# Performance work log

Hardware: AMD Instinct MI355X
Metric: run time of the kernel (lower is better)

Reference implementation:

```python
import jax, jax.numpy as jnp
import numpy as np

B, L, H, V = 16, 1024, 512, 32000
HALF = H // 2
ALPHA = 0.95
EPS_NORM = 1e-12
EPS_LN = 1e-5


def setup_inputs() -> dict:
    key = jax.random.key(0)
    ks = jax.random.split(key, 12)
    s = 0.02
    return {
        "seq": jax.random.randint(ks[0], (B, L), 0, V),
        "embed": jax.random.normal(ks[1], (V, H), jnp.float32) * s,
        "ff_w1": jax.random.normal(ks[2], (2 * H, H), jnp.float32) * s,
        "ff_b1": jnp.zeros((2 * H,), jnp.float32),
        "ff_w2": jax.random.normal(ks[3], (H, 2 * H), jnp.float32) * s,
        "ff_b2": jnp.zeros((H,), jnp.float32),
        "gamma": jnp.ones((H,), jnp.float32),
        "beta": jnp.zeros((H,), jnp.float32),
        "sem_w": jax.random.normal(ks[4], (HALF, H), jnp.float32) * s,
        "epi_w": jax.random.normal(ks[5], (HALF, H), jnp.float32) * s,
        "rp_w": jax.random.normal(ks[6], (H, H), jnp.float32) * s,
        "rp_b": jnp.zeros((H,), jnp.float32),
        "out_w": jax.random.normal(ks[7], (V, H), jnp.float32) * s,
        "out_b": jnp.zeros((V,), jnp.float32),
    }


def _layernorm(x, gamma, beta):
    mu = jnp.mean(x, axis=-1, keepdims=True)
    var = jnp.mean(jnp.square(x - mu), axis=-1, keepdims=True)
    return (x - mu) * jax.lax.rsqrt(var + EPS_LN) * gamma + beta


def _l2norm(k):
    # F.normalize: k / max(||k||_2, eps)
    n = jnp.sqrt(jnp.sum(jnp.square(k), axis=-1, keepdims=True))
    return k / jnp.maximum(n, EPS_NORM)


def reference(seq, embed, ff_w1, ff_b1, ff_w2, ff_b2, gamma, beta,
              sem_w, epi_w, rp_w, rp_b, out_w, out_b):
    h = embed[seq]  # [B, L, H]
    ff = jnp.maximum(jnp.einsum('blh,fh->blf', h, ff_w1) + ff_b1, 0.0)
    ff = jnp.einsum('blf,hf->blh', ff, ff_w2) + ff_b2
    h = _layernorm(h + ff, gamma, beta)  # [B, L, H]

    # precompute all keys, time-major for scan: [L, B, half]
    ks_all = jnp.einsum('blh,ch->lbc', h, sem_w)
    ke_all = jnp.einsum('blh,ch->lbc', h, epi_w)

    def step(carry, inp):
        Ms, Me = carry                      # [B, half, half]
        ks, ke = inp                        # [B, half]
        kns = _l2norm(ks)
        kne = _l2norm(ke)
        vps = jnp.einsum('bij,bj->bi', Ms, kns)
        vpe = jnp.einsum('bij,bj->bi', Me, kne)
        Ds = (ks - vps)[:, :, None] * kns[:, None, :]
        De = (ke - vpe)[:, :, None] * kne[:, None, :]
        Ms = Ms + (1.0 - ALPHA) * Ds
        Me = Me + (1.0 - ALPHA) * De
        return (Ms, Me), None

    M0 = jnp.zeros((B, HALF, HALF), h.dtype)
    (M_s, M_e), _ = jax.lax.scan(step, (M0, M0), (ks_all[:L - 1], ke_all[:L - 1]))

    qs = ks_all[L - 1]  # sem_p(h[:, -1])
    qe = ke_all[L - 1]  # epi_p(h[:, -1])
    cs = jnp.einsum('bij,bj->bi', M_s, qs)
    ce = jnp.einsum('bij,bj->bi', M_e, qe)
    c = jnp.concatenate([cs, ce], axis=-1)  # [B, H]
    r = jnp.einsum('bh,gh->bg', c, rp_w) + rp_b
    return jnp.einsum('bh,vh->bv', r, out_w) + out_b  # [B, V]
```

## Files before the change

### kernel.cpp

```cpp
#include <hip/hip_runtime.h>
#include <stdint.h>

#define Bsz 16
#define Lsz 1024
#define Hsz 512
#define Vsz 32000
#define HALF 256
#define BETA 0.05f

typedef unsigned short u16;
typedef __attribute__((ext_vector_type(8))) short short8;
typedef __attribute__((ext_vector_type(4))) float f32x4;

__device__ __forceinline__ float bf2f(u16 u) { return __uint_as_float(((unsigned int)u) << 16); }
__device__ __forceinline__ u16 f2bf(float f) {
    unsigned int u = __float_as_uint(f);
    return (u16)((u + 0x7FFFu + ((u >> 16) & 1u)) >> 16);
}
__device__ __forceinline__ u16 f2h(float f) {
    _Float16 h = (_Float16)f;
    return *(u16*)&h;
}
__device__ __forceinline__ bool mode_f32(const void* gamma) {
    return *(const unsigned int*)gamma == 0x3F800000u;
}

__device__ __forceinline__ float wave_sum(float p) {
    p += __shfl_xor(p, 32, 64);
    p += __shfl_xor(p, 16, 64);
    p += __shfl_xor(p, 8, 64);
    p += __shfl_xor(p, 4, 64);
    p += __shfl_xor(p, 2, 64);
    p += __shfl_xor(p, 1, 64);
    return p;
}

__device__ __forceinline__ void cvt8(const void* src, u16* dst, int i, bool f32m) {
    union { u16 u[8]; uint4 q; } o;
    if (f32m) {
        const float* s = (const float*)src + i;
        const float4 a = *(const float4*)s;
        const float4 b = *(const float4*)(s + 4);
        o.u[0] = f2bf(a.x); o.u[1] = f2bf(a.y); o.u[2] = f2bf(a.z); o.u[3] = f2bf(a.w);
        o.u[4] = f2bf(b.x); o.u[5] = f2bf(b.y); o.u[6] = f2bf(b.z); o.u[7] = f2bf(b.w);
    } else {
        o.q = *(const uint4*)((const u16*)src + i);
    }
    *(uint4*)(dst + i) = o.q;
}

__global__ __launch_bounds__(256)
void cvt_all(const void* s0, const void* s1, const void* s2, const void* s3,
             const void* s4, const void* s5, const void* s6, const void* s7,
             const void* s8, const void* s9, const void* s10,
             u16* d0, u16* d1, u16* d2, u16* d3, u16* d4, u16* d5, u16* d6,
             u16* d7, u16* d8, u16* d9, u16* d10, const void* gamma) {
    const bool f32m = mode_f32(gamma);
    const int g = blockIdx.x * 256 + threadIdx.x;
    const void* src; u16* dst; int off;
    if      (g < 65536)  { src = s0;  dst = d0;  off = g; }
    else if (g < 131072) { src = s1;  dst = d1;  off = g - 65536; }
    else if (g < 147456) { src = s2;  dst = d2;  off = g - 131072; }
    else if (g < 163840) { src = s3;  dst = d3;  off = g - 147456; }
    else if (g < 196608) { src = s4;  dst = d4;  off = g - 163840; }
    else if (g < 196736) { src = s5;  dst = d5;  off = g - 196608; }
    else if (g < 196800) { src = s6;  dst = d6;  off = g - 196736; }
    else if (g < 196864) { src = s7;  dst = d7;  off = g - 196800; }
    else if (g < 196928) { src = s8;  dst = d8;  off = g - 196864; }
    else if (g < 196992) { src = s9;  dst = d9;  off = g - 196928; }
    else if (g < 200992) { src = s10; dst = d10; off = g - 196992; }
    else return;
    cvt8(src, dst, off * 8, f32m);
}

__global__ __launch_bounds__(256)
void gather_kernel(const int* __restrict__ seq, const void* __restrict__ embed,
                   u16* __restrict__ h0, const void* __restrict__ gamma) {
    const bool f32m = mode_f32(gamma);
    const int row = blockIdx.x * 4 + (threadIdx.x >> 6);
    const int lane = threadIdx.x & 63;
    const int tok = seq[row];
    union { u16 u[8]; uint4 q; } o;
    if (f32m) {
        const float* e = (const float*)embed + (size_t)tok * Hsz + lane * 8;
        const float4 a = *(const float4*)e;
        const float4 b = *(const float4*)(e + 4);
        o.u[0] = f2bf(a.x); o.u[1] = f2bf(a.y); o.u[2] = f2bf(a.z); o.u[3] = f2bf(a.w);
        o.u[4] = f2bf(b.x); o.u[5] = f2bf(b.y); o.u[6] = f2bf(b.z); o.u[7] = f2bf(b.w);
    } else {
        o.q = *((const uint4*)((const u16*)embed + (size_t)tok * Hsz) + lane);
    }
    *((uint4*)(h0 + (size_t)row * Hsz) + lane) = o.q;
}

template <int EPI>
__global__ __launch_bounds__(256)
void gemm128(const u16* __restrict__ A, const u16* __restrict__ B0,
             const u16* __restrict__ B1, const u16* __restrict__ bias,
             const u16* resid, void* Cout, u16* __restrict__ kT,
             int M, int N, int K) {
    __shared__ u16 Als[128 * 32];
    __shared__ u16 Bls[128 * 32];
    const int tid = threadIdx.x;
    const int wave = tid >> 6, lane = tid & 63;
    const int m0 = blockIdx.y * 128, n0 = blockIdx.x * 128;

    const u16* Bt;
    if (EPI == 2) Bt = (n0 < HALF) ? (B0 + (size_t)n0 * K) : (B1 + (size_t)(n0 - HALF) * K);
    else          Bt = B0 + (size_t)n0 * K;
    const u16* At = A + (size_t)m0 * K;

    const int wm = wave >> 1, wn = wave & 1;
    const int srow = lane >> 2;
    const int sk = (lane & 3) * 8;
    const int fr = lane & 15;
    const int fq = (lane >> 4) * 8;

    f32x4 acc[4][4];
#pragma unroll
    for (int i = 0; i < 4; i++)
#pragma unroll
        for (int j = 0; j < 4; j++) acc[i][j] = (f32x4){0.f, 0.f, 0.f, 0.f};

    for (int k0 = 0; k0 < K; k0 += 32) {
        __syncthreads();
#pragma unroll
        for (int c = 0; c < 2; c++) {
            const int ch = wave * 2 + c;
            const int row = ch * 16 + srow;
            __builtin_amdgcn_global_load_lds(
                (const __attribute__((address_space(1))) uint32_t*)(At + (size_t)row * K + k0 + sk),
                (__attribute__((address_space(3))) uint32_t*)(&Als[ch * 512]), 16, 0, 0);
            __builtin_amdgcn_global_load_lds(
                (const __attribute__((address_space(1))) uint32_t*)(Bt + (size_t)row * K + k0 + sk),
                (__attribute__((address_space(3))) uint32_t*)(&Bls[ch * 512]), 16, 0, 0);
        }
        __syncthreads();
        short8 af[4], bfr[4];
#pragma unroll
        for (int i = 0; i < 4; i++)
            af[i] = *(const short8*)&Als[(wm * 64 + i * 16 + fr) * 32 + fq];
#pragma unroll
        for (int j = 0; j < 4; j++)
            bfr[j] = *(const short8*)&Bls[(wn * 64 + j * 16 + fr) * 32 + fq];
#pragma unroll
        for (int i = 0; i < 4; i++)
#pragma unroll
            for (int j = 0; j < 4; j++)
                acc[i][j] = __builtin_amdgcn_mfma_f32_16x16x32_bf16(af[i], bfr[j], acc[i][j], 0, 0, 0);
    }

#pragma unroll
    for (int i = 0; i < 4; i++) {
#pragma unroll
        for (int j = 0; j < 4; j++) {
            const int n = n0 + wn * 64 + j * 16 + fr;
            if (EPI == 2) {
                const int mbase = m0 + wm * 64 + i * 16 + (lane >> 4) * 4;
                const int mem = n >> 8, col = n & 255;
                const int b = mbase >> 10, t0 = mbase & 1023;
                u16 tv[4];
#pragma unroll
                for (int r = 0; r < 4; r++) {
                    const int t = t0 + r;
                    const u16 bv = f2bf(acc[i][j][r]);
                    tv[r] = bv;
                    ((u16*)Cout)[((size_t)(mem * Bsz + b) * Lsz + t) * HALF + col] = bv;
                }
                *(uint2*)&kT[((size_t)(mem * Bsz + b) * HALF + col) * Lsz + t0] = *(uint2*)tv;
            } else {
#pragma unroll
                for (int r = 0; r < 4; r++) {
                    const int m = m0 + wm * 64 + i * 16 + (lane >> 4) * 4 + r;
                    float v = acc[i][j][r];
                    if (EPI == 0) {
                        v += bf2f(bias[n]);
                        v = v > 0.f ? v : 0.f;
                        ((u16*)Cout)[(size_t)m * N + n] = f2bf(v);
                    } else {
                        v += bf2f(bias[n]) + bf2f(resid[(size_t)m * N + n]);
                        ((u16*)Cout)[(size_t)m * N + n] = f2bf(v);
                    }
                }
            }
        }
    }
}

__global__ __launch_bounds__(256)
void ln_kernel(const u16* hs, const u16* __restrict__ gamma,
               const u16* __restrict__ beta, u16* hn) {
    const int row = blockIdx.x * 4 + (threadIdx.x >> 6);
    const int lane = threadIdx.x & 63;
    const uint4 raw = *(const uint4*)(hs + (size_t)row * Hsz + lane * 8);
    const u16* xr = (const u16*)&raw;
    float v[8];
#pragma unroll
    for (int j = 0; j < 8; j++) v[j] = bf2f(xr[j]);
    float s = 0.f;
#pragma unroll
    for (int j = 0; j < 8; j++) s += v[j];
    s = wave_sum(s);
    const float mu = s * (1.f / 512.f);
    float q = 0.f;
#pragma unroll
    for (int j = 0; j < 8; j++) { v[j] -= mu; q += v[j] * v[j]; }
    q = wave_sum(q);
    const float rstd = rsqrtf(q * (1.f / 512.f) + 1e-5f);
    union { u16 u[8]; uint4 qv; } o;
#pragma unroll
    for (int j = 0; j < 8; j++) {
        const int n = lane * 8 + j;
        o.u[j] = f2bf(v[j] * rstd * bf2f(gamma[n]) + bf2f(beta[n]));
    }
    *(uint4*)(hn + (size_t)row * Hsz + lane * 8) = o.qv;
}

__global__ __launch_bounds__(256)
void normalize_kernel(u16* kb, float* __restrict__ norms, float* __restrict__ invs) {
    const int row = blockIdx.x * 4 + (threadIdx.x >> 6);
    const int lane = threadIdx.x & 63;
    u16* p = kb + (size_t)row * HALF + lane * 4;
    uint2 raw = *(uint2*)p;
    const u16* kp = (const u16*)&raw;
    float f[4];
#pragma unroll
    for (int j = 0; j < 4; j++) f[j] = bf2f(kp[j]);
    float s = f[0]*f[0] + f[1]*f[1] + f[2]*f[2] + f[3]*f[3];
    s = wave_sum(s);
    const float n = fmaxf(sqrtf(s), 1e-12f);
    const float inv = 1.f / n;
    union { u16 u[4]; uint2 q; } o;
#pragma unroll
    for (int j = 0; j < 4; j++) o.u[j] = f2bf(f[j] * inv);
    *(uint2*)p = o.q;
    if (lane == 0) { norms[row] = n; invs[row] = inv; }
}

__global__ __launch_bounds__(256)
void gramsolve_kernel(const u16* __restrict__ kn, u16* __restrict__ W) {
    __shared__ u16 ls[64 * 264];
    __shared__ float Gl[64 * 64];
    const int mb = blockIdx.x, c = blockIdx.y;
    const int tid = threadIdx.x;
    const u16* src = kn + ((size_t)mb * Lsz + c * 64) * HALF;
    {
        const int row = tid >> 2, p = tid & 3;
        const u16* sp = src + row * 256 + p * 64;
        u16* dp = ls + row * 264 + p * 64;
#pragma unroll
        for (int i = 0; i < 8; i++)
            *(uint4*)(dp + i * 8) = *(const uint4*)(sp + i * 8);
    }
    __syncthreads();
    const int wave = tid >> 6, lane = tid & 63;
    const int fr = lane & 15, fq = (lane >> 4) * 8;
    f32x4 acc[4];
#pragma unroll
    for (int j = 0; j < 4; j++) acc[j] = (f32x4){0.f, 0.f, 0.f, 0.f};
    for (int k0 = 0; k0 < 256; k0 += 32) {
        const short8 a = *(const short8*)&ls[(wave * 16 + fr) * 264 + k0 + fq];
#pragma unroll
        for (int j = 0; j < 4; j++) {
            const short8 b = *(const short8*)&ls[(j * 16 + fr) * 264 + k0 + fq];
            acc[j] = __builtin_amdgcn_mfma_f32_16x16x32_bf16(a, b, acc[j], 0, 0, 0);
        }
    }
#pragma unroll
    for (int j = 0; j < 4; j++)
#pragma unroll
        for (int r = 0; r < 4; r++)
            Gl[(wave * 16 + (lane >> 4) * 4 + r) * 64 + j * 16 + fr] = acc[j][r];
    __syncthreads();

    u16* Wc = W + (((size_t)mb * 16 + c) * 64) * HALF;
    const bool last = (c == 15);
    float w[64];
#pragma unroll
    for (int t = 63; t >= 0; --t) {
        float a0 = 0.f, a1 = 0.f, a2 = 0.f, a3 = 0.f;
        const int q0 = (t + 4) & ~3;
#pragma unroll
        for (int tp = t + 1; tp < q0; ++tp) a0 += Gl[t * 64 + tp] * w[tp];
#pragma unroll
        for (int q = q0; q < 64; q += 4) {
            const f32x4 g = *(const f32x4*)&Gl[t * 64 + q];
            a0 += g[0] * w[q];     a1 += g[1] * w[q + 1];
            a2 += g[2] * w[q + 2]; a3 += g[3] * w[q + 3];
        }
        float wt = bf2f(ls[t * 264 + tid]) - BETA * ((a0 + a1) + (a2 + a3));
        if (last && t == 63) wt = 0.f;
        w[t] = wt;
        Wc[t * HALF + tid] = f2h(wt);
    }
}

__global__ __launch_bounds__(256, 1)
void scan3_kernel(const u16* __restrict__ kn, const u16* __restrict__ kT,
                  const float* __restrict__ norms, const float* __restrict__ invs,
                  const u16* __restrict__ W, float* __restrict__ cbuf) {
    __shared__ float uL[256], suL[64], scL[64];
    const int mb = blockIdx.x;
    const int tid = threadIdx.x;
    const int t = tid >> 2, p = tid & 3;
    const float* nb = norms + (size_t)mb * Lsz;
    const float* ib = invs + (size_t)mb * Lsz;

    float u = bf2f(kn[((size_t)mb * Lsz + 1023) * HALF + tid]) * nb[1023];
    float cacc = 0.f;
    uL[tid] = u;

    const u16* kTrow = kT + ((size_t)mb * HALF + tid) * Lsz;
    const u16* Wrow = W + (size_t)mb * 16 * 64 * HALF + (size_t)t * HALF + (size_t)p * 64;

    uint4 wA[8], kA[8], wB[8], kB[8];
    {
        const u16* wp = Wrow + (size_t)15 * 64 * HALF;
        const u16* kp = kTrow + 15 * 64;
#pragma unroll
        for (int i = 0; i < 8; i++) wA[i] = *(const uint4*)(wp + i * 8);
#pragma unroll
        for (int i = 0; i < 8; i++) kA[i] = *(const uint4*)(kp + i * 8);
    }
    asm volatile("s_waitcnt lgkmcnt(0)" ::: "memory");
    __builtin_amdgcn_s_barrier();

    auto process = [&](const uint4 (&WR)[8], const uint4 (&KQ)[8], const int c) {
        {
            float pa = 0.f, pb = 0.f;
#pragma unroll
            for (int i = 0; i < 8; i++) {
                union { uint4 q; _Float16 h[8]; } wv; wv.q = WR[i];
                const f32x4 u0 = *(const f32x4*)&uL[p * 64 + i * 8];
                const f32x4 u1 = *(const f32x4*)&uL[p * 64 + i * 8 + 4];
                pa += (float)wv.h[0] * u0[0] + (float)wv.h[1] * u0[1]
                    + (float)wv.h[2] * u0[2] + (float)wv.h[3] * u0[3];
                pb += (float)wv.h[4] * u1[0] + (float)wv.h[5] * u1[1]
                    + (float)wv.h[6] * u1[2] + (float)wv.h[7] * u1[3];
            }
            float part = pa + pb;
            part += __shfl_xor(part, 1, 64);
            part += __shfl_xor(part, 2, 64);
            if (p == 0) { suL[t] = part * ib[c * 64 + t]; scL[t] = part; }
        }
        asm volatile("s_waitcnt lgkmcnt(0)" ::: "memory");
        __builtin_amdgcn_s_barrier();
        {
            float du0 = 0.f, du1 = 0.f, dc0 = 0.f, dc1 = 0.f;
#pragma unroll
            for (int i = 0; i < 8; i++) {
                const u16* kk = (const u16*)&KQ[i];
                const f32x4 sa = *(const f32x4*)&suL[i * 8];
                const f32x4 sb = *(const f32x4*)&suL[i * 8 + 4];
                const f32x4 ca = *(const f32x4*)&scL[i * 8];
                const f32x4 cb = *(const f32x4*)&scL[i * 8 + 4];
                const float k0 = bf2f(kk[0]), k1 = bf2f(kk[1]);
                const float k2 = bf2f(kk[2]), k3 = bf2f(kk[3]);
                const float k4 = bf2f(kk[4]), k5 = bf2f(kk[5]);
                const float k6 = bf2f(kk[6]), k7 = bf2f(kk[7]);
                du0 += sa[0] * k0 + sa[1] * k1 + sa[2] * k2 + sa[3] * k3;
                du1 += sb[0] * k4 + sb[1] * k5 + sb[2] * k6 + sb[3] * k7;
                dc0 += ca[0] * k0 + ca[1] * k1 + ca[2] * k2 + ca[3] * k3;
                dc1 += cb[0] * k4 + cb[1] * k5 + cb[2] * k6 + cb[3] * k7;
            }
            u -= BETA * (du0 + du1);
            cacc += BETA * (dc0 + dc1);
            uL[tid] = u;
        }
        asm volatile("s_waitcnt lgkmcnt(0)" ::: "memory");
        __builtin_amdgcn_s_barrier();
    };

    for (int cc = 15; cc >= 1; cc -= 2) {
        {
            const u16* wp = Wrow + (size_t)(cc - 1) * 64 * HALF;
            const u16* kp = kTrow + (cc - 1) * 64;
#pragma unroll
            for (int i = 0; i < 8; i++) wB[i] = *(const uint4*)(wp + i * 8);
#pragma unroll
            for (int i = 0; i < 8; i++) kB[i] = *(const uint4*)(kp + i * 8);
        }
        __builtin_amdgcn_sched_barrier(0);
        process(wA, kA, cc);
        if (cc >= 3) {
            const u16* wp = Wrow + (size_t)(cc - 2) * 64 * HALF;
            const u16* kp = kTrow + (cc - 2) * 64;
#pragma unroll
            for (int i = 0; i < 8; i++) wA[i] = *(const uint4*)(wp + i * 8);
#pragma unroll
            for (int i = 0; i < 8; i++) kA[i] = *(const uint4*)(kp + i * 8);
        }
        __builtin_amdgcn_sched_barrier(0);
        process(wB, kB, cc - 1);
    }
    const int b = mb & 15, mem = mb >> 4;
    cbuf[(size_t)b * Hsz + mem * HALF + tid] = cacc;
}

__global__ __launch_bounds__(256)
void rproj_kernel(const float* __restrict__ cbuf, const u16* __restrict__ rpw,
                  const u16* __restrict__ rpb, u16* __restrict__ rbuf) {
    __shared__ float cl[Hsz];
    const int b = blockIdx.x, tid = threadIdx.x;
    cl[tid] = cbuf[(size_t)b * Hsz + tid];
    cl[tid + 256] = cbuf[(size_t)b * Hsz + 256 + tid];
    __syncthreads();
#pragma unroll
    for (int gg = 0; gg < 2; gg++) {
        const int g = gg * 256 + tid;
        const u16* wr = rpw + (size_t)g * Hsz;
        float acc = bf2f(rpb[g]);
        for (int k = 0; k < Hsz; k += 8) {
            const uint4 w8 = *(const uint4*)(wr + k);
            const u16* w = (const u16*)&w8;
            const float4 c0 = *(const float4*)&cl[k];
            const float4 c1 = *(const float4*)&cl[k + 4];
            acc += bf2f(w[0]) * c0.x + bf2f(w[1]) * c0.y + bf2f(w[2]) * c0.z + bf2f(w[3]) * c0.w
                 + bf2f(w[4]) * c1.x + bf2f(w[5]) * c1.y + bf2f(w[6]) * c1.z + bf2f(w[7]) * c1.w;
        }
        rbuf[(size_t)b * Hsz + g] = f2bf(acc);
    }
}

__global__ __launch_bounds__(256)
void logits_kernel(const u16* __restrict__ rbuf, const void* __restrict__ outw,
                   const u16* __restrict__ outb, void* __restrict__ out,
                   const void* __restrict__ gamma) {
    __shared__ u16 rls[16 * Hsz];
    const bool f32m = mode_f32(gamma);
    const int tid = threadIdx.x;
    {
        const uint4* src = (const uint4*)rbuf;
        uint4* dst = (uint4*)rls;
#pragma unroll
        for (int i = 0; i < 4; i++) dst[i * 256 + tid] = src[i * 256 + tid];
    }
    __syncthreads();
    const int wave = tid >> 6, lane = tid & 63;
    const int n0 = blockIdx.x * 256 + wave * 64;
    const int fr = lane & 15, fq = (lane >> 4) * 8;
    f32x4 acc[4];
#pragma unroll
    for (int j = 0; j < 4; j++) acc[j] = (f32x4){0.f, 0.f, 0.f, 0.f};
    if (f32m) {
        for (int k0 = 0; k0 < Hsz; k0 += 32) {
            const short8 af = *(const short8*)&rls[fr * Hsz + k0 + fq];
#pragma unroll
            for (int j = 0; j < 4; j++) {
                const float* wp = (const float*)outw + (size_t)(n0 + j * 16 + fr) * Hsz + k0 + fq;
                const float4 a = *(const float4*)wp;
                const float4 bq = *(const float4*)(wp + 4);
                union { u16 u[8]; short8 v; } bb;
                bb.u[0] = f2bf(a.x); bb.u[1] = f2bf(a.y); bb.u[2] = f2bf(a.z); bb.u[3] = f2bf(a.w);
                bb.u[4] = f2bf(bq.x); bb.u[5] = f2bf(bq.y); bb.u[6] = f2bf(bq.z); bb.u[7] = f2bf(bq.w);
                acc[j] = __builtin_amdgcn_mfma_f32_16x16x32_bf16(af, bb.v, acc[j], 0, 0, 0);
            }
        }
    } else {
        for (int k0 = 0; k0 < Hsz; k0 += 32) {
            const short8 af = *(const short8*)&rls[fr * Hsz + k0 + fq];
#pragma unroll
            for (int j = 0; j < 4; j++) {
                const short8 b8 = *(const short8*)((const u16*)outw + (size_t)(n0 + j * 16 + fr) * Hsz + k0 + fq);
                acc[j] = __builtin_amdgcn_mfma_f32_16x16x32_bf16(af, b8, acc[j], 0, 0, 0);
            }
        }
    }
#pragma unroll
    for (int j = 0; j < 4; j++) {
        const int v = n0 + j * 16 + fr;
        const float bv = bf2f(outb[v]);
#pragma unroll
        for (int r = 0; r < 4; r++) {
            const int bb = (lane >> 4) * 4 + r;
            const float val = acc[j][r] + bv;
            if (f32m) ((float*)out)[(size_t)bb * Vsz + v] = val;
            else      ((u16*)out)[(size_t)bb * Vsz + v] = f2bf(val);
        }
    }
}

extern "C" void kernel_launch(void* const* d_in, const int* in_sizes, int n_in,
                              void* d_out, int out_size, void* d_ws, size_t ws_size,
                              hipStream_t stream) {
    const int*  seq   = (const int*)d_in[0];
    const void* embed = d_in[1];
    const void* ffw1  = d_in[2];
    const void* ffb1  = d_in[3];
    const void* ffw2  = d_in[4];
    const void* ffb2  = d_in[5];
    const void* gamma = d_in[6];
    const void* beta  = d_in[7];
    const void* semw  = d_in[8];
    const void* epiw  = d_in[9];
    const void* rpw   = d_in[10];
    const void* rpb   = d_in[11];
    const void* outw  = d_in[12];
    const void* outb  = d_in[13];

    char* ws = (char*)d_ws;
    u16*   h0    = (u16*)(ws + 0);
    u16*   Wbuf  = (u16*)(ws + 0);
    u16*   C1    = (u16*)(ws + (size_t)0x1000000);
    u16*   kbuf  = (u16*)(ws + (size_t)0x1000000);
    u16*   kT    = (u16*)(ws + (size_t)0x2000000);
    size_t off   = 50331648;
    float* norms = (float*)(ws + off); off += (size_t)32 * Lsz * 4;
    float* invs  = (float*)(ws + off); off += (size_t)32 * Lsz * 4;
    u16* cffw1 = (u16*)(ws + off); off += (size_t)1024 * 512 * 2;
    u16* cffw2 = (u16*)(ws + off); off += (size_t)512 * 1024 * 2;
    u16* csemw = (u16*)(ws + off); off += (size_t)256 * 512 * 2;
    u16* cepiw = (u16*)(ws + off); off += (size_t)256 * 512 * 2;
    u16* crpw  = (u16*)(ws + off); off += (size_t)512 * 512 * 2;
    u16* cffb1 = (u16*)(ws + off); off += 1024 * 2;
    u16* cffb2 = (u16*)(ws + off); off += 512 * 2;
    u16* cgam  = (u16*)(ws + off); off += 512 * 2;
    u16* cbet  = (u16*)(ws + off); off += 512 * 2;
    u16* crpb  = (u16*)(ws + off); off += 512 * 2;
    u16* coutb = (u16*)(ws + off); off += (size_t)32000 * 2;
    off = (off + 255) & ~(size_t)255;
    float* cbuf = (float*)(ws + off); off += (size_t)16 * 512 * 4;
    u16*   rbuf = (u16*)(ws + off);

    cvt_all<<<786, 256, 0, stream>>>(ffw1, ffw2, semw, epiw, rpw, ffb1, ffb2,
                                     gamma, beta, rpb, outb,
                                     cffw1, cffw2, csemw, cepiw, crpw, cffb1, cffb2,
                                     cgam, cbet, crpb, coutb, gamma);
    gather_kernel<<<4096, 256, 0, stream>>>(seq, embed, h0, gamma);
    gemm128<0><<<dim3(8, 128), 256, 0, stream>>>(h0, cffw1, nullptr, cffb1, nullptr, C1,
                                                 nullptr, 16384, 1024, 512);
    gemm128<1><<<dim3(4, 128), 256, 0, stream>>>(C1, cffw2, nullptr, cffb2, h0, h0,
                                                 nullptr, 16384, 512, 1024);
    ln_kernel<<<4096, 256, 0, stream>>>(h0, cgam, cbet, h0);
    gemm128<2><<<dim3(4, 128), 256, 0, stream>>>(h0, csemw, cepiw, nullptr, nullptr, kbuf,
                                                 kT, 16384, 512, 512);
    normalize_kernel<<<8192, 256, 0, stream>>>(kbuf, norms, invs);
    gramsolve_kernel<<<dim3(32, 16), 256, 0, stream>>>(kbuf, Wbuf);
    scan3_kernel<<<32, 256, 0, stream>>>(kbuf, kT, norms, invs, Wbuf, cbuf);
    rproj_kernel<<<16, 256, 0, stream>>>(cbuf, crpw, crpb, rbuf);
    logits_kernel<<<125, 256, 0, stream>>>(rbuf, outw, coutb, d_out, gamma);
}
```

Baseline: 385.0 us.

## Tile kT and W buffers so scan3 loads are fully coalesced

Changes the global layout of the transposed key buffer and the per-chunk W buffer to a blocked format: chunk, 8-element group, column, 8 elements. In this format each thread's 16-byte loads in the scan kernel are contiguous across the block. The W producer now stages its results through shared memory and writes them out as coalesced uint4 stores. The GEMM epilogue writes kT in the same tiled order. The aim is to replace strided per-thread row reads in the latency-bound scan with coalesced accesses, at the cost of an extra LDS staging pass and two barriers in the W kernel.

```diff
diff --git a/kernel.cpp b/kernel.cpp
--- a/kernel.cpp
+++ b/kernel.cpp
@@ -167,7 +167,11 @@
                     tv[r] = bv;
                     ((u16*)Cout)[((size_t)(mem * Bsz + b) * Lsz + t) * HALF + col] = bv;
                 }
-                *(uint2*)&kT[((size_t)(mem * Bsz + b) * HALF + col) * Lsz + t0] = *(uint2*)tv;
+                const size_t kaddr = (size_t)(mem * Bsz + b) * 262144
+                                   + (size_t)(t0 >> 6) * 16384
+                                   + (size_t)((t0 >> 3) & 7) * 2048
+                                   + (size_t)col * 8 + (t0 & 7);
+                *(uint2*)&kT[kaddr] = *(uint2*)tv;
             } else {
 #pragma unroll
                 for (int r = 0; r < 4; r++) {
@@ -273,7 +277,6 @@
             Gl[(wave * 16 + (lane >> 4) * 4 + r) * 64 + j * 16 + fr] = acc[j][r];
     __syncthreads();
 
-    u16* Wc = W + (((size_t)mb * 16 + c) * 64) * HALF;
     const bool last = (c == 15);
     float w[64];
 #pragma unroll
@@ -291,8 +294,19 @@
         float wt = bf2f(ls[t * 264 + tid]) - BETA * ((a0 + a1) + (a2 + a3));
         if (last && t == 63) wt = 0.f;
         w[t] = wt;
-        Wc[t * HALF + tid] = f2h(wt);
-    }
+    }
+    __syncthreads();
+    {
+        const int i_ = (tid >> 3) & 7, p_ = tid >> 6, e_ = tid & 7;
+#pragma unroll
+        for (int t = 0; t < 64; t++)
+            ls[i_ * 2056 + (t * 4 + p_) * 8 + e_] = f2h(w[t]);
+    }
+    __syncthreads();
+    u16* Wc = W + ((size_t)mb * 16 + c) * 16384;
+#pragma unroll
+    for (int i2 = 0; i2 < 8; i2++)
+        *(uint4*)(Wc + i2 * 2048 + tid * 8) = *(const uint4*)(ls + i2 * 2056 + tid * 8);
 }
 
 __global__ __launch_bounds__(256, 1)
@@ -310,17 +324,17 @@
     float cacc = 0.f;
     uL[tid] = u;
 
-    const u16* kTrow = kT + ((size_t)mb * HALF + tid) * Lsz;
-    const u16* Wrow = W + (size_t)mb * 16 * 64 * HALF + (size_t)t * HALF + (size_t)p * 64;
+    const u16* kTmb = kT + (size_t)mb * 262144;
+    const u16* Wmb  = W  + (size_t)mb * 262144;
 
     uint4 wA[8], kA[8], wB[8], kB[8];
     {
-        const u16* wp = Wrow + (size_t)15 * 64 * HALF;
-        const u16* kp = kTrow + 15 * 64;
-#pragma unroll
-        for (int i = 0; i < 8; i++) wA[i] = *(const uint4*)(wp + i * 8);
-#pragma unroll
-        for (int i = 0; i < 8; i++) kA[i] = *(const uint4*)(kp + i * 8);
+        const u16* wp = Wmb + (size_t)15 * 16384;
+        const u16* kp = kTmb + (size_t)15 * 16384;
+#pragma unroll
+        for (int i = 0; i < 8; i++) wA[i] = *(const uint4*)(wp + i * 2048 + tid * 8);
+#pragma unroll
+        for (int i = 0; i < 8; i++) kA[i] = *(const uint4*)(kp + i * 2048 + tid * 8);
     }
     asm volatile("s_waitcnt lgkmcnt(0)" ::: "memory");
     __builtin_amdgcn_s_barrier();
@@ -373,22 +387,22 @@
 
     for (int cc = 15; cc >= 1; cc -= 2) {
         {
-            const u16* wp = Wrow + (size_t)(cc - 1) * 64 * HALF;
-            const u16* kp = kTrow + (cc - 1) * 64;
-#pragma unroll
-            for (int i = 0; i < 8; i++) wB[i] = *(const uint4*)(wp + i * 8);
-#pragma unroll
-            for (int i = 0; i < 8; i++) kB[i] = *(const uint4*)(kp + i * 8);
+            const u16* wp = Wmb + (size_t)(cc - 1) * 16384;
+            const u16* kp = kTmb + (size_t)(cc - 1) * 16384;
+#pragma unroll
+            for (int i = 0; i < 8; i++) wB[i] = *(const uint4*)(wp + i * 2048 + tid * 8);
+#pragma unroll
+            for (int i = 0; i < 8; i++) kB[i] = *(const uint4*)(kp + i * 2048 + tid * 8);
         }
         __builtin_amdgcn_sched_barrier(0);
         process(wA, kA, cc);
         if (cc >= 3) {
-            const u16* wp = Wrow + (size_t)(cc - 2) * 64 * HALF;
-            const u16* kp = kTrow + (cc - 2) * 64;
-#pragma unroll
-            for (int i = 0; i < 8; i++) wA[i] = *(const uint4*)(wp + i * 8);
-#pragma unroll
-            for (int i = 0; i < 8; i++) kA[i] = *(const uint4*)(kp + i * 8);
+            const u16* wp = Wmb + (size_t)(cc - 2) * 16384;
+            const u16* kp = kTmb + (size_t)(cc - 2) * 16384;
+#pragma unroll
+            for (int i = 0; i < 8; i++) wA[i] = *(const uint4*)(wp + i * 2048 + tid * 8);
+#pragma unroll
+            for (int i = 0; i < 8; i++) kA[i] = *(const uint4*)(kp + i * 2048 + tid * 8);
         }
         __builtin_amdgcn_sched_barrier(0);
         process(wB, kB, cc - 1);
```

Result: faster. 372.6 us (-3.2%).
